# Performance work log

Measured on AMD Instinct MI355X. Metric: run time of the kernel, lower is better.

Reference implementation:

```python
import jax, jax.numpy as jnp
import numpy as np

T_LEN = 1024
N_IN = 512
BATCH = 32
SURR_ALPHA = 4.0  # slope of the sigmoid surrogate gradient


@jax.custom_vjp
def heaviside_sg(x):
    # spike = Heaviside(x); backward uses sigmoid surrogate derivative
    return (x >= 0).astype(x.dtype)

def _hs_fwd(x):
    return heaviside_sg(x), x

def _hs_bwd(x, g):
    s = jax.nn.sigmoid(SURR_ALPHA * x)
    return (g * SURR_ALPHA * s * (1.0 - s),)

heaviside_sg.defvjp(_hs_fwd, _hs_bwd)


def setup_inputs() -> dict:
    key = jax.random.key(0)
    k1, k2, k3 = jax.random.split(key, 3)
    current = jax.random.normal(k1, (T_LEN, BATCH, N_IN), dtype=jnp.float32)
    beta = jax.random.uniform(k2, (N_IN,), dtype=jnp.float32)  # per-channel decay in (0,1)
    v_init = jax.random.normal(k3, (BATCH, N_IN), dtype=jnp.float32)
    v_th = jnp.ones((T_LEN, BATCH, N_IN), dtype=jnp.float32)
    return {"current": current, "beta": beta, "v_init": v_init, "v_th": v_th}


def reference(current, beta, v_init, v_th):
    # Torch version: grouped causal conv1d with kernel beta^{T-1-k}, i.e.
    # membrane[t] = sum_{j<=t} beta^{t-j} * current[j], with current[0] += beta*v_init.
    # Equivalent O(T) linear recurrence: m_t = beta*m_{t-1} + c_t, m_{-1}=v_init.
    def step(m, c):
        m = beta * m + c  # beta (N,) broadcasts over (B,N)
        return m, m

    m_last, membrane = jax.lax.scan(step, v_init, current)  # membrane: (T,B,N)

    # surrogate-gradient spike function
    spikes = heaviside_sg(membrane - v_th)  # (T,B,N)

    # triangular phi kernel: z[t] = sum_{j<=t} (t-j+1)*spikes[j] == double cumsum
    z = jnp.cumsum(jnp.cumsum(spikes, axis=0), axis=0)  # (T,B,N)

    # Block.g: keep entries equal to 1, zero everything else; gradient is identity
    # (the subtracted term is detached in the torch code).
    gz = z - jax.lax.stop_gradient(jnp.where(z == 1.0, 0.0, z))

    return gz, z, m_last  # m_last == membrane[:, :, -1] in torch layout (B,N)
```

## Files before the change

kernel.cpp:

```cpp
#include <hip/hip_runtime.h>


#define T_LEN 1024
#define N_IN  512
#define BN    16384
#define U     16

struct Buf { float c[U]; float v[U]; };

__device__ __forceinline__ void prefetch(Buf& b, const float* __restrict__ cp,
                                         const float* __restrict__ vp, int t0) {
    const float* __restrict__ c = cp + t0 * BN;
    const float* __restrict__ v = vp + t0 * BN;
#pragma unroll
    for (int u = 0; u < U; ++u) {
        b.c[u] = c[u * BN];
        b.v[u] = v[u * BN];
    }
}

__device__ __forceinline__ void process(const Buf& b, float beta, float& m, int& c1,
                                        int& z, float* __restrict__ gp,
                                        float* __restrict__ zp, int t0) {
#pragma unroll
    for (int u = 0; u < U; ++u) {
        m = fmaf(beta, m, b.c[u]);
        c1 += (m >= b.v[u]) ? 1 : 0;
        z  += c1;
        gp[(t0 + u) * BN] = (z == 1) ? 1.0f : 0.0f;
        zp[(t0 + u) * BN] = (float)z;
    }
}

__global__ __launch_bounds__(64, 1) void snn_scan(
        const float* __restrict__ cur, const float* __restrict__ beta,
        const float* __restrict__ vini, const float* __restrict__ vth,
        float* __restrict__ gz, float* __restrict__ zo, float* __restrict__ ml)
{
    const int i = blockIdx.x * 64 + threadIdx.x;
    const float bta = beta[i & (N_IN - 1)];
    float m = vini[i];
    int c1 = 0, z = 0;

    const float* cp = cur + i;
    const float* vp = vth + i;
    float* gp = gz + i;
    float* zp = zo + i;

    Buf b0, b1, b2, b3;
    prefetch(b0, cp, vp, 0);
    prefetch(b1, cp, vp, U);
    prefetch(b2, cp, vp, 2 * U);
    prefetch(b3, cp, vp, 3 * U);

    for (int t0 = 0; t0 < T_LEN; t0 += 4 * U) {
        process(b0, bta, m, c1, z, gp, zp, t0);
        if (t0 + 4 * U < T_LEN) prefetch(b0, cp, vp, t0 + 4 * U);
        process(b1, bta, m, c1, z, gp, zp, t0 + U);
        if (t0 + 5 * U < T_LEN) prefetch(b1, cp, vp, t0 + 5 * U);
        process(b2, bta, m, c1, z, gp, zp, t0 + 2 * U);
        if (t0 + 6 * U < T_LEN) prefetch(b2, cp, vp, t0 + 6 * U);
        process(b3, bta, m, c1, z, gp, zp, t0 + 3 * U);
        if (t0 + 7 * U < T_LEN) prefetch(b3, cp, vp, t0 + 7 * U);
    }
    ml[i] = m;
}

extern "C" void kernel_launch(void* const* d_in, const int* in_sizes, int n_in,
                              void* d_out, int out_size, void* d_ws, size_t ws_size,
                              hipStream_t stream) {
    const float* cur  = (const float*)d_in[0];
    const float* beta = (const float*)d_in[1];
    const float* vini = (const float*)d_in[2];
    const float* vth  = (const float*)d_in[3];
    float* gz = (float*)d_out;
    float* zo = gz + (size_t)T_LEN * BN;
    float* ml = zo + (size_t)T_LEN * BN;
    snn_scan<<<BN / 64, 64, 0, stream>>>(cur, beta, vini, vth, gz, zo, ml);
}
```

Before: 250.1 us.

## Stream inputs through an LDS ring buffer via async global_load_lds

Replaces the register-based 4x16 prefetch buffers with asynchronous global-to-LDS loads into a 6-slot ring of 8-timestep chunks, kept 4 chunks ahead. A manual s_waitcnt vmcnt threshold stands in for the compiler's conservative waits. The aim is to keep more loads in flight with fewer registers on this low-occupancy, bandwidth-bound scan. In exchange it relies on the vmcnt counting being correct, since stores also count toward vmcnt, and it adds LDS round-trips.

```diff
diff --git a/kernel.cpp b/kernel.cpp
--- a/kernel.cpp
+++ b/kernel.cpp
@@ -1,69 +1,69 @@
 #include <hip/hip_runtime.h>
+#include <stdint.h>
 
 
-#define T_LEN 1024
-#define N_IN  512
-#define BN    16384
-#define U     16
+#define T_LEN  1024
+#define N_IN   512
+#define BN     16384
+#define CT     8
+#define NCHUNK (T_LEN / CT)
+#define NSLOT  6
+#define DEPTH  4
 
-struct Buf { float c[U]; float v[U]; };
-
-__device__ __forceinline__ void prefetch(Buf& b, const float* __restrict__ cp,
-                                         const float* __restrict__ vp, int t0) {
-    const float* __restrict__ c = cp + t0 * BN;
-    const float* __restrict__ v = vp + t0 * BN;
-#pragma unroll
-    for (int u = 0; u < U; ++u) {
-        b.c[u] = c[u * BN];
-        b.v[u] = v[u * BN];
-    }
-}
-
-__device__ __forceinline__ void process(const Buf& b, float beta, float& m, int& c1,
-                                        int& z, float* __restrict__ gp,
-                                        float* __restrict__ zp, int t0) {
-#pragma unroll
-    for (int u = 0; u < U; ++u) {
-        m = fmaf(beta, m, b.c[u]);
-        c1 += (m >= b.v[u]) ? 1 : 0;
-        z  += c1;
-        gp[(t0 + u) * BN] = (z == 1) ? 1.0f : 0.0f;
-        zp[(t0 + u) * BN] = (float)z;
-    }
-}
+#define AS_GLOBAL(p) (const __attribute__((address_space(1))) void*)(p)
+#define AS_LDS(p)    (__attribute__((address_space(3))) void*)(p)
 
 __global__ __launch_bounds__(64, 1) void snn_scan(
         const float* __restrict__ cur, const float* __restrict__ beta,
         const float* __restrict__ vini, const float* __restrict__ vth,
         float* __restrict__ gz, float* __restrict__ zo, float* __restrict__ ml)
 {
-    const int i = blockIdx.x * 64 + threadIdx.x;
-    const float bta = beta[i & (N_IN - 1)];
-    float m = vini[i];
+    __shared__ float bc[NSLOT][CT][64];
+    __shared__ float bv[NSLOT][CT][64];
+
+    const int tid = threadIdx.x;
+    const int ch  = blockIdx.x * 64 + tid;
+    const float bta = beta[ch & (N_IN - 1)];
+    float m = vini[ch];
     int c1 = 0, z = 0;
 
-    const float* cp = cur + i;
-    const float* vp = vth + i;
-    float* gp = gz + i;
-    float* zp = zo + i;
+    const float* cp = cur + ch;
+    const float* vp = vth + ch;
+    float* gp = gz + ch;
+    float* zp = zo + ch;
 
-    Buf b0, b1, b2, b3;
-    prefetch(b0, cp, vp, 0);
-    prefetch(b1, cp, vp, U);
-    prefetch(b2, cp, vp, 2 * U);
-    prefetch(b3, cp, vp, 3 * U);
+    auto issue = [&](int chunk) {
+        const int slot = chunk % NSLOT;
+        const float* c0 = cp + (size_t)chunk * CT * BN;
+        const float* v0 = vp + (size_t)chunk * CT * BN;
+#pragma unroll
+        for (int t = 0; t < CT; ++t) {
+            __builtin_amdgcn_global_load_lds(AS_GLOBAL(c0 + (size_t)t * BN),
+                                             AS_LDS(&bc[slot][t][0]), 4, 0, 0);
+            __builtin_amdgcn_global_load_lds(AS_GLOBAL(v0 + (size_t)t * BN),
+                                             AS_LDS(&bv[slot][t][0]), 4, 0, 0);
+        }
+    };
 
-    for (int t0 = 0; t0 < T_LEN; t0 += 4 * U) {
-        process(b0, bta, m, c1, z, gp, zp, t0);
-        if (t0 + 4 * U < T_LEN) prefetch(b0, cp, vp, t0 + 4 * U);
-        process(b1, bta, m, c1, z, gp, zp, t0 + U);
-        if (t0 + 5 * U < T_LEN) prefetch(b1, cp, vp, t0 + 5 * U);
-        process(b2, bta, m, c1, z, gp, zp, t0 + 2 * U);
-        if (t0 + 6 * U < T_LEN) prefetch(b2, cp, vp, t0 + 6 * U);
-        process(b3, bta, m, c1, z, gp, zp, t0 + 3 * U);
-        if (t0 + 7 * U < T_LEN) prefetch(b3, cp, vp, t0 + 7 * U);
+    issue(0); issue(1); issue(2); issue(3);
+
+    for (int chunk = 0; chunk < NCHUNK; ++chunk) {
+        if (chunk + DEPTH < NCHUNK) issue(chunk + DEPTH);
+        asm volatile("s_waitcnt vmcnt(48)" ::: "memory");
+        const int slot = chunk % NSLOT;
+#pragma unroll
+        for (int t = 0; t < CT; ++t) {
+            const float c = bc[slot][t][tid];
+            const float v = bv[slot][t][tid];
+            m = fmaf(bta, m, c);
+            c1 += (m >= v) ? 1 : 0;
+            z  += c1;
+            const size_t off = (size_t)(chunk * CT + t) * BN;
+            gp[off] = (z == 1) ? 1.0f : 0.0f;
+            zp[off] = (float)z;
+        }
     }
-    ml[i] = m;
+    ml[ch] = m;
 }
 
 extern "C" void kernel_launch(void* const* d_in, const int* in_sizes, int n_in,
```

After: 312.7 us. 25.0% more time.
